# Performance work log

Hardware: AMD Instinct MI355X
Metric: run time of the kernel (lower is better)

The kernel has to match this reference:

```python
import jax, jax.numpy as jnp
import numpy as np

B, N, K, C, D, DP = 4, 4096, 32, 3, 64, 128  # batch, npoint, nsample, xyz, feat, all_channel
DC = C + D + 2  # channels of dgf = pg|pf|dg|df
ALPHA = 0.2


def setup_inputs() -> dict:
    key = jax.random.key(0)
    ks = jax.random.split(key, 10)
    g = jax.random.normal(ks[0], (B, N, C), jnp.float32)
    f = jax.random.normal(ks[1], (B, N, D), jnp.float32)
    gn = jax.random.normal(ks[2], (B, N, K, C), jnp.float32)
    fn = jax.random.normal(ks[3], (B, N, K, D), jnp.float32)
    nfn = jax.random.normal(ks[4], (B, N, K, DP), jnp.float32)
    # learned params: attention matrix a (xavier-uniform in torch), 1x1 conv2d (DC->DP), 1x1 conv1d (DP->DP)
    lim_a = float(1.414 * np.sqrt(6.0 / (DP + DP)))
    a = jax.random.uniform(ks[5], (DP, DP), jnp.float32, -lim_a, lim_a)
    w2 = jax.random.normal(ks[6], (DC, DP), jnp.float32) * 0.05
    b2 = jax.random.normal(ks[7], (DP,), jnp.float32) * 0.01
    w1 = jax.random.normal(ks[8], (DP, DP), jnp.float32) * 0.05
    b1 = jax.random.normal(ks[9], (DP,), jnp.float32) * 0.01
    return {"g": g, "f": f, "gn": gn, "fn": fn, "nfn": nfn,
            "a": a, "w2": w2, "b2": b2, "w1": w1, "b1": b1,
            "b": B, "n": N, "k": K, "c": DP, "nc": DP}


def reference(g, f, gn, fn, nfn, a, w2, b2, w1, b1, b, n, k, c, nc):
    # relative coords / features: [B,N,K,C], [B,N,K,D]
    pg = g[:, :, None, :] - gn
    pf = f[:, :, None, :] - fn
    # diso(A, B) = sqrt(sum((A-B)^2, -1))[..., None]
    dg = jnp.sqrt(jnp.sum((pg - gn) ** 2, axis=-1, keepdims=True))  # [B,N,K,1]
    df = jnp.sqrt(jnp.sum((pf - fn) ** 2, axis=-1, keepdims=True))  # [B,N,K,1]
    dgf = jnp.concatenate([pg, pf, dg, df], axis=-1)                 # [B,N,K,DC]
    # 1x1 conv2d projection (computed but unused by the original forward; returned here)
    disf = jnp.einsum("bnkd,de->bnke", dgf, w2) + b2                # [B,N,K,DP]
    # GAT-style attention over the neighbor axis
    e = jax.nn.leaky_relu(jnp.einsum("bnkd,de->bnke", nfn, a), ALPHA)
    att = jax.nn.softmax(e, axis=2)  # softmax over nsample; dropout is identity in eval mode
    pooled = jnp.sum(att * nfn, axis=2)                              # [B,N,DP]
    out = jnp.einsum("bnd,dc->bnc", pooled, w1) + b1                 # [B,N,c]
    return out, disf
```

## Files before the change

kernel.cpp:

```cpp
#include <hip/hip_runtime.h>
#include <math.h>

constexpr int Bv = 4;
constexpr int Nv = 4096;
constexpr int Kv = 32;
constexpr int Cv = 3;
constexpr int Dv = 64;
constexpr int DP = 128;
constexpr float ALPHA = 0.2f;

typedef __bf16 bf16x8 __attribute__((ext_vector_type(8)));
typedef float  f32x4  __attribute__((ext_vector_type(4)));
typedef short  s16x8  __attribute__((ext_vector_type(8)));

__device__ __forceinline__ short f2bf(float x) {
    unsigned u = __float_as_uint(x);
    unsigned r = (u + 0x7FFFu + ((u >> 16) & 1u)) >> 16;
    return (short)r;
}
__device__ __forceinline__ float bf2f(short s) {
    return __uint_as_float(((unsigned)(unsigned short)s) << 16);
}
__device__ __forceinline__ int swz(int row, int bytecol) {
    return row * 256 + (bytecol ^ ((row & 7) << 4));
}
__device__ __forceinline__ bf16x8 ld_frag(const char* base, int row, int bytecol) {
    return __builtin_bit_cast(bf16x8, *(const s16x8*)(base + swz(row, bytecol)));
}

__global__ __launch_bounds__(256) void prep_kernel(
    const float* __restrict__ a, const float* __restrict__ w2,
    const float* __restrict__ w1,
    short* __restrict__ aT_swz, short* __restrict__ w2T_swz,
    float* __restrict__ w1T)
{
    const int idx = blockIdx.x * 256 + threadIdx.x;
    const int c = idx >> 7, s = idx & 127;
    const int off = (c * 256 + ((s * 2) ^ ((c & 7) << 4))) >> 1;
    aT_swz[off] = f2bf(a[(size_t)s * DP + c]);
    float v = 0.f;
    if (s < 64)       v = w2[(size_t)(3 + s) * DP + c];
    else if (s < 67)  v = w2[(size_t)(s - 64) * DP + c];
    else if (s == 67) v = w2[(size_t)67 * DP + c];
    else if (s == 68) v = w2[(size_t)68 * DP + c];
    w2T_swz[off] = f2bf(v);
    w1T[(size_t)c * DP + s] = w1[(size_t)s * DP + c];
}

__global__ __launch_bounds__(256, 2) void attn_kernel(
    const float* __restrict__ nfn,
    const short* __restrict__ aT_swz,
    const float* __restrict__ w1T,
    const float* __restrict__ b1,
    float* __restrict__ out)
{
    __shared__ __align__(16) char s_nfn[128 * 256];
    __shared__ __align__(16) char s_aT[128 * 256];
    __shared__ float s_pool[4][DP];

    const int bn0 = blockIdx.x * 4;
    const int t = threadIdx.x;

    {
        const s16x8* src = (const s16x8*)aT_swz;
        s16x8* dst = (s16x8*)s_aT;
#pragma unroll
        for (int i = 0; i < 8; ++i) dst[t + 256 * i] = src[t + 256 * i];
    }
    {
        const int r = t >> 1, h = t & 1;
        const float4* src = (const float4*)(nfn + ((size_t)bn0 * 32 + r) * DP + h * 64);
#pragma unroll
        for (int cc = 0; cc < 8; ++cc) {
            float4 v0 = src[2 * cc], v1 = src[2 * cc + 1];
            s16x8 v = { f2bf(v0.x), f2bf(v0.y), f2bf(v0.z), f2bf(v0.w),
                        f2bf(v1.x), f2bf(v1.y), f2bf(v1.z), f2bf(v1.w) };
            *(s16x8*)(s_nfn + swz(r, h * 128 + cc * 16)) = v;
        }
    }
    __syncthreads();

    const int w = t >> 6, lane = t & 63;
    const int wr = w >> 1, wc = w & 1;
    const int lg = lane >> 4, lm = lane & 15;

    f32x4 acc[4][4];
#pragma unroll
    for (int mt = 0; mt < 4; ++mt)
#pragma unroll
        for (int nt = 0; nt < 4; ++nt) acc[mt][nt] = (f32x4)0.f;

#pragma unroll
    for (int kt = 0; kt < 4; ++kt) {
        bf16x8 afr[4], bfr[4];
#pragma unroll
        for (int mt = 0; mt < 4; ++mt)
            afr[mt] = ld_frag(s_nfn, wr * 64 + mt * 16 + lm, kt * 64 + lg * 16);
#pragma unroll
        for (int nt = 0; nt < 4; ++nt)
            bfr[nt] = ld_frag(s_aT, wc * 64 + nt * 16 + lm, kt * 64 + lg * 16);
#pragma unroll
        for (int mt = 0; mt < 4; ++mt)
#pragma unroll
            for (int nt = 0; nt < 4; ++nt)
                acc[mt][nt] = __builtin_amdgcn_mfma_f32_16x16x32_bf16(
                    afr[mt], bfr[nt], acc[mt][nt], 0, 0, 0);
    }

#pragma unroll
    for (int gp = 0; gp < 2; ++gp) {
#pragma unroll
        for (int nt = 0; nt < 4; ++nt) {
            float v[8];
            float m = -1e30f;
#pragma unroll
            for (int tt = 0; tt < 2; ++tt)
#pragma unroll
                for (int rg = 0; rg < 4; ++rg) {
                    float e = acc[2 * gp + tt][nt][rg];
                    e = e > 0.f ? e : ALPHA * e;
                    v[tt * 4 + rg] = e;
                    m = fmaxf(m, e);
                }
            m = fmaxf(m, __shfl_xor(m, 16));
            m = fmaxf(m, __shfl_xor(m, 32));
            float s = 0.f, p = 0.f;
            const int col = wc * 64 + nt * 16 + lm;
#pragma unroll
            for (int tt = 0; tt < 2; ++tt)
#pragma unroll
                for (int rg = 0; rg < 4; ++rg) {
                    float ex = __expf(v[tt * 4 + rg] - m);
                    s += ex;
                    const int row = wr * 64 + (2 * gp + tt) * 16 + lg * 4 + rg;
                    p += ex * bf2f(*(const short*)(s_nfn + swz(row, col * 2)));
                }
            s += __shfl_xor(s, 16); s += __shfl_xor(s, 32);
            p += __shfl_xor(p, 16); p += __shfl_xor(p, 32);
            if (lg == 0) s_pool[wr * 2 + gp][col] = p / s;
        }
    }
    __syncthreads();

    {
        const int c = t & 127, g2 = t >> 7;
        const float4* w1r = (const float4*)(w1T + (size_t)c * DP);
#pragma unroll
        for (int gg = 0; gg < 2; ++gg) {
            const int g = g2 + 2 * gg;
            const float4* pr = (const float4*)(&s_pool[g][0]);
            float acc2 = b1[c];
#pragma unroll
            for (int j = 0; j < 32; ++j) {
                float4 wv = w1r[j];
                float4 pv = pr[j];
                acc2 = fmaf(pv.x, wv.x, acc2);
                acc2 = fmaf(pv.y, wv.y, acc2);
                acc2 = fmaf(pv.z, wv.z, acc2);
                acc2 = fmaf(pv.w, wv.w, acc2);
            }
            out[((size_t)bn0 + g) * DP + c] = acc2;
        }
    }
}

__global__ __launch_bounds__(256, 2) void disf_kernel(
    const float* __restrict__ g,
    const float* __restrict__ f,
    const float* __restrict__ gn,
    const float* __restrict__ fn,
    const short* __restrict__ w2T_swz,
    const float* __restrict__ b2,
    float* __restrict__ disf)
{
    __shared__ __align__(16) char s_dgf[128 * 256];
    __shared__ __align__(16) char s_w2T[128 * 256];

    const int bn0 = blockIdx.x * 4;
    const int t = threadIdx.x;

    {
        const s16x8* src = (const s16x8*)w2T_swz;
        s16x8* dst = (s16x8*)s_w2T;
#pragma unroll
        for (int i = 0; i < 8; ++i) dst[t + 256 * i] = src[t + 256 * i];
    }
    {
        const int r = t >> 1, h = t & 1;
        const int grp = r >> 5, k = r & 31;
        const size_t bn = bn0 + grp;
        const float4* fp  = (const float4*)(f + bn * Dv + h * 32);
        const float4* fnp = (const float4*)(fn + (bn * Kv + k) * Dv + h * 32);
        float sq = 0.f;
#pragma unroll
        for (int cc = 0; cc < 4; ++cc) {
            float4 f0 = fp[2 * cc],  f1 = fp[2 * cc + 1];
            float4 n0 = fnp[2 * cc], n1 = fnp[2 * cc + 1];
            float p0 = f0.x - n0.x, p1 = f0.y - n0.y, p2 = f0.z - n0.z, p3 = f0.w - n0.w;
            float p4 = f1.x - n1.x, p5 = f1.y - n1.y, p6 = f1.z - n1.z, p7 = f1.w - n1.w;
            float q;
            q = p0 - n0.x; sq += q * q;  q = p1 - n0.y; sq += q * q;
            q = p2 - n0.z; sq += q * q;  q = p3 - n0.w; sq += q * q;
            q = p4 - n1.x; sq += q * q;  q = p5 - n1.y; sq += q * q;
            q = p6 - n1.z; sq += q * q;  q = p7 - n1.w; sq += q * q;
            s16x8 v = { f2bf(p0), f2bf(p1), f2bf(p2), f2bf(p3),
                        f2bf(p4), f2bf(p5), f2bf(p6), f2bf(p7) };
            *(s16x8*)(s_dgf + swz(r, h * 64 + cc * 16)) = v;
        }
        sq += __shfl_xor(sq, 1);
        if (h == 0) {
            const float* gp  = g + bn * Cv;
            const float* gnp = gn + (bn * Kv + k) * Cv;
            float p0 = gp[0] - gnp[0], p1 = gp[1] - gnp[1], p2 = gp[2] - gnp[2];
            float q0 = p0 - gnp[0], q1 = p1 - gnp[1], q2 = p2 - gnp[2];
            float dg = sqrtf(q0 * q0 + q1 * q1 + q2 * q2);
            float df = sqrtf(sq);
            s16x8 z = (s16x8)(short)0;
            s16x8 head = z;
            head[0] = f2bf(p0); head[1] = f2bf(p1); head[2] = f2bf(p2);
            head[3] = f2bf(dg); head[4] = f2bf(df);
            *(s16x8*)(s_dgf + swz(r, 128)) = head;
            *(s16x8*)(s_dgf + swz(r, 144)) = z;
            *(s16x8*)(s_dgf + swz(r, 160)) = z;
            *(s16x8*)(s_dgf + swz(r, 176)) = z;
        }
    }
    __syncthreads();

    const int w = t >> 6, lane = t & 63;
    const int wr = w >> 1, wc = w & 1;
    const int lg = lane >> 4, lm = lane & 15;

    f32x4 acc[4][4];
#pragma unroll
    for (int mt = 0; mt < 4; ++mt)
#pragma unroll
        for (int nt = 0; nt < 4; ++nt) acc[mt][nt] = (f32x4)0.f;

#pragma unroll
    for (int kt = 0; kt < 3; ++kt) {
        bf16x8 afr[4], bfr[4];
#pragma unroll
        for (int mt = 0; mt < 4; ++mt)
            afr[mt] = ld_frag(s_dgf, wr * 64 + mt * 16 + lm, kt * 64 + lg * 16);
#pragma unroll
        for (int nt = 0; nt < 4; ++nt)
            bfr[nt] = ld_frag(s_w2T, wc * 64 + nt * 16 + lm, kt * 64 + lg * 16);
#pragma unroll
        for (int mt = 0; mt < 4; ++mt)
#pragma unroll
            for (int nt = 0; nt < 4; ++nt)
                acc[mt][nt] = __builtin_amdgcn_mfma_f32_16x16x32_bf16(
                    afr[mt], bfr[nt], acc[mt][nt], 0, 0, 0);
    }

    float b2v[4];
#pragma unroll
    for (int nt = 0; nt < 4; ++nt) b2v[nt] = b2[wc * 64 + nt * 16 + lm];

#pragma unroll
    for (int mt = 0; mt < 4; ++mt) {
#pragma unroll
        for (int rg = 0; rg < 4; ++rg) {
            const int row = wr * 64 + mt * 16 + lg * 4 + rg;
            float* dst = disf + ((size_t)bn0 * 32 + row) * DP + wc * 64 + lm;
#pragma unroll
            for (int nt = 0; nt < 4; ++nt)
                dst[nt * 16] = acc[mt][nt][rg] + b2v[nt];
        }
    }
}

extern "C" void kernel_launch(void* const* d_in, const int* in_sizes, int n_in,
                              void* d_out, int out_size, void* d_ws, size_t ws_size,
                              hipStream_t stream) {
    (void)in_sizes; (void)n_in; (void)out_size; (void)ws_size;

    const float* g   = (const float*)d_in[0];
    const float* f   = (const float*)d_in[1];
    const float* gn  = (const float*)d_in[2];
    const float* fn  = (const float*)d_in[3];
    const float* nfn = (const float*)d_in[4];
    const float* a   = (const float*)d_in[5];
    const float* w2  = (const float*)d_in[6];
    const float* b2  = (const float*)d_in[7];
    const float* w1  = (const float*)d_in[8];
    const float* b1  = (const float*)d_in[9];

    float* out  = (float*)d_out;
    float* disf = out + (size_t)Bv * Nv * DP;

    short* aT_swz  = (short*)d_ws;
    short* w2T_swz = aT_swz + 128 * 128;
    float* w1T     = (float*)(w2T_swz + 128 * 128);

    prep_kernel<<<64, 256, 0, stream>>>(a, w2, w1, aT_swz, w2T_swz, w1T);

    dim3 grid(Bv * Nv / 4);
    attn_kernel<<<grid, 256, 0, stream>>>(nfn, aT_swz, w1T, b1, out);
    disf_kernel<<<grid, 256, 0, stream>>>(g, f, gn, fn, w2T_swz, b2, disf);
}
```

Measured before the change: 802.5 us.

## Restructure attention and disf kernels to per-wave 32x32 MFMA with register prefetch

Each wave now processes one neighbor group at a time using 32x32x16 bf16 MFMAs and prefetches the next group's inputs into registers while computing the current one, replacing block-wide 16x16 tiles and a sync. The output projection is split into a separate MFMA kernel that reads pooled features staged in a scratch region carved from the tail of the disf output buffer. The projection now runs in bf16 instead of fp32 FMAs. This aims to overlap global loads with compute and reduce LDS traffic, but adds a kernel launch and a dependency on disf_kernel overwriting the scratch later.

```diff
diff --git a/kernel.cpp b/kernel.cpp
--- a/kernel.cpp
+++ b/kernel.cpp
@@ -8,10 +8,12 @@
 constexpr int Dv = 64;
 constexpr int DP = 128;
 constexpr float ALPHA = 0.2f;
+constexpr int NG = Bv * Nv;
 
 typedef __bf16 bf16x8 __attribute__((ext_vector_type(8)));
-typedef float  f32x4  __attribute__((ext_vector_type(4)));
+typedef float  f32x16 __attribute__((ext_vector_type(16)));
 typedef short  s16x8  __attribute__((ext_vector_type(8)));
+typedef short  s16x4  __attribute__((ext_vector_type(4)));
 
 __device__ __forceinline__ short f2bf(float x) {
     unsigned u = __float_as_uint(x);
@@ -32,34 +34,31 @@
     const float* __restrict__ a, const float* __restrict__ w2,
     const float* __restrict__ w1,
     short* __restrict__ aT_swz, short* __restrict__ w2T_swz,
-    float* __restrict__ w1T)
+    short* __restrict__ w1T_swz)
 {
     const int idx = blockIdx.x * 256 + threadIdx.x;
     const int c = idx >> 7, s = idx & 127;
     const int off = (c * 256 + ((s * 2) ^ ((c & 7) << 4))) >> 1;
-    aT_swz[off] = f2bf(a[(size_t)s * DP + c]);
+    aT_swz[off]  = f2bf(a[(size_t)s * DP + c]);
+    w1T_swz[off] = f2bf(w1[(size_t)s * DP + c]);
     float v = 0.f;
     if (s < 64)       v = w2[(size_t)(3 + s) * DP + c];
     else if (s < 67)  v = w2[(size_t)(s - 64) * DP + c];
     else if (s == 67) v = w2[(size_t)67 * DP + c];
     else if (s == 68) v = w2[(size_t)68 * DP + c];
     w2T_swz[off] = f2bf(v);
-    w1T[(size_t)c * DP + s] = w1[(size_t)s * DP + c];
-}
-
-__global__ __launch_bounds__(256, 2) void attn_kernel(
+}
+
+__global__ __launch_bounds__(256, 2) void attn_core(
     const float* __restrict__ nfn,
     const short* __restrict__ aT_swz,
-    const float* __restrict__ w1T,
-    const float* __restrict__ b1,
-    float* __restrict__ out)
+    float* __restrict__ pooled)
 {
-    __shared__ __align__(16) char s_nfn[128 * 256];
     __shared__ __align__(16) char s_aT[128 * 256];
-    __shared__ float s_pool[4][DP];
-
-    const int bn0 = blockIdx.x * 4;
-    const int t = threadIdx.x;
+    __shared__ __align__(16) char s_buf[4][32 * 256];
+
+    const int t = threadIdx.x, w = t >> 6, l = t & 63;
+    const int lg = l >> 5, lG = l & 31;
 
     {
         const s16x8* src = (const s16x8*)aT_swz;
@@ -67,101 +66,128 @@
 #pragma unroll
         for (int i = 0; i < 8; ++i) dst[t + 256 * i] = src[t + 256 * i];
     }
-    {
-        const int r = t >> 1, h = t & 1;
-        const float4* src = (const float4*)(nfn + ((size_t)bn0 * 32 + r) * DP + h * 64);
-#pragma unroll
-        for (int cc = 0; cc < 8; ++cc) {
-            float4 v0 = src[2 * cc], v1 = src[2 * cc + 1];
-            s16x8 v = { f2bf(v0.x), f2bf(v0.y), f2bf(v0.z), f2bf(v0.w),
-                        f2bf(v1.x), f2bf(v1.y), f2bf(v1.z), f2bf(v1.w) };
-            *(s16x8*)(s_nfn + swz(r, h * 128 + cc * 16)) = v;
-        }
-    }
     __syncthreads();
 
-    const int w = t >> 6, lane = t & 63;
-    const int wr = w >> 1, wc = w & 1;
-    const int lg = lane >> 4, lm = lane & 15;
-
-    f32x4 acc[4][4];
-#pragma unroll
-    for (int mt = 0; mt < 4; ++mt)
-#pragma unroll
-        for (int nt = 0; nt < 4; ++nt) acc[mt][nt] = (f32x4)0.f;
-
-#pragma unroll
-    for (int kt = 0; kt < 4; ++kt) {
-        bf16x8 afr[4], bfr[4];
-#pragma unroll
-        for (int mt = 0; mt < 4; ++mt)
-            afr[mt] = ld_frag(s_nfn, wr * 64 + mt * 16 + lm, kt * 64 + lg * 16);
-#pragma unroll
-        for (int nt = 0; nt < 4; ++nt)
-            bfr[nt] = ld_frag(s_aT, wc * 64 + nt * 16 + lm, kt * 64 + lg * 16);
-#pragma unroll
-        for (int mt = 0; mt < 4; ++mt)
-#pragma unroll
-            for (int nt = 0; nt < 4; ++nt)
-                acc[mt][nt] = __builtin_amdgcn_mfma_f32_16x16x32_bf16(
-                    afr[mt], bfr[nt], acc[mt][nt], 0, 0, 0);
-    }
-
-#pragma unroll
-    for (int gp = 0; gp < 2; ++gp) {
+    char* buf = s_buf[w];
+    const int g0 = blockIdx.x * 16 + w * 4;
+
+    float4 rv[16];
+    {
+        const float4* src = (const float4*)(nfn + (size_t)g0 * Kv * DP);
+#pragma unroll
+        for (int j = 0; j < 16; ++j) rv[j] = src[j * 64 + l];
+    }
+
+    for (int it = 0; it < 4; ++it) {
+        const int g = g0 + it;
+#pragma unroll
+        for (int j = 0; j < 16; ++j) {
+            s16x4 v = { f2bf(rv[j].x), f2bf(rv[j].y), f2bf(rv[j].z), f2bf(rv[j].w) };
+            *(s16x4*)(buf + swz(j * 2 + lg, lG * 8)) = v;
+        }
+        if (it < 3) {
+            const float4* src = (const float4*)(nfn + (size_t)(g + 1) * Kv * DP);
+#pragma unroll
+            for (int j = 0; j < 16; ++j) rv[j] = src[j * 64 + l];
+        }
+
+        bf16x8 afr[8];
+#pragma unroll
+        for (int k = 0; k < 8; ++k) afr[k] = ld_frag(buf, lG, k * 32 + lg * 16);
+
+        f32x16 acc[4];
+#pragma unroll
+        for (int nt = 0; nt < 4; ++nt) acc[nt] = (f32x16)0.f;
+#pragma unroll
+        for (int k = 0; k < 8; ++k)
+#pragma unroll
+            for (int nt = 0; nt < 4; ++nt) {
+                bf16x8 bfr = ld_frag(s_aT, nt * 32 + lG, k * 32 + lg * 16);
+                acc[nt] = __builtin_amdgcn_mfma_f32_32x32x16_bf16(
+                    afr[k], bfr, acc[nt], 0, 0, 0);
+            }
+
 #pragma unroll
         for (int nt = 0; nt < 4; ++nt) {
-            float v[8];
+            float v[16];
             float m = -1e30f;
 #pragma unroll
-            for (int tt = 0; tt < 2; ++tt)
-#pragma unroll
-                for (int rg = 0; rg < 4; ++rg) {
-                    float e = acc[2 * gp + tt][nt][rg];
-                    e = e > 0.f ? e : ALPHA * e;
-                    v[tt * 4 + rg] = e;
-                    m = fmaxf(m, e);
-                }
-            m = fmaxf(m, __shfl_xor(m, 16));
+            for (int r = 0; r < 16; ++r) {
+                float e = acc[nt][r];
+                e = e > 0.f ? e : ALPHA * e;
+                v[r] = e;
+                m = fmaxf(m, e);
+            }
             m = fmaxf(m, __shfl_xor(m, 32));
             float s = 0.f, p = 0.f;
-            const int col = wc * 64 + nt * 16 + lm;
-#pragma unroll
-            for (int tt = 0; tt < 2; ++tt)
-#pragma unroll
-                for (int rg = 0; rg < 4; ++rg) {
-                    float ex = __expf(v[tt * 4 + rg] - m);
-                    s += ex;
-                    const int row = wr * 64 + (2 * gp + tt) * 16 + lg * 4 + rg;
-                    p += ex * bf2f(*(const short*)(s_nfn + swz(row, col * 2)));
-                }
-            s += __shfl_xor(s, 16); s += __shfl_xor(s, 32);
-            p += __shfl_xor(p, 16); p += __shfl_xor(p, 32);
-            if (lg == 0) s_pool[wr * 2 + gp][col] = p / s;
-        }
+            const int col = nt * 32 + lG;
+#pragma unroll
+            for (int r = 0; r < 16; ++r) {
+                float ex = __expf(v[r] - m);
+                s += ex;
+                const int row = (r & 3) + 8 * (r >> 2) + 4 * lg;
+                p += ex * bf2f(*(const short*)(buf + swz(row, col * 2)));
+            }
+            s += __shfl_xor(s, 32);
+            p += __shfl_xor(p, 32);
+            if (lg == 0) pooled[(size_t)g * DP + col] = p / s;
+        }
+    }
+}
+
+__global__ __launch_bounds__(256, 2) void out_proj(
+    const float* __restrict__ pooled, const short* __restrict__ w1T_swz,
+    const float* __restrict__ b1, float* __restrict__ out)
+{
+    __shared__ __align__(16) char s_w1[128 * 256];
+    __shared__ __align__(16) char s_buf[4][32 * 256];
+
+    const int t = threadIdx.x, w = t >> 6, l = t & 63;
+    const int lg = l >> 5, lG = l & 31;
+    {
+        const s16x8* src = (const s16x8*)w1T_swz;
+        s16x8* dst = (s16x8*)s_w1;
+#pragma unroll
+        for (int i = 0; i < 8; ++i) dst[t + 256 * i] = src[t + 256 * i];
     }
     __syncthreads();
 
-    {
-        const int c = t & 127, g2 = t >> 7;
-        const float4* w1r = (const float4*)(w1T + (size_t)c * DP);
-#pragma unroll
-        for (int gg = 0; gg < 2; ++gg) {
-            const int g = g2 + 2 * gg;
-            const float4* pr = (const float4*)(&s_pool[g][0]);
-            float acc2 = b1[c];
-#pragma unroll
-            for (int j = 0; j < 32; ++j) {
-                float4 wv = w1r[j];
-                float4 pv = pr[j];
-                acc2 = fmaf(pv.x, wv.x, acc2);
-                acc2 = fmaf(pv.y, wv.y, acc2);
-                acc2 = fmaf(pv.z, wv.z, acc2);
-                acc2 = fmaf(pv.w, wv.w, acc2);
-            }
-            out[((size_t)bn0 + g) * DP + c] = acc2;
-        }
-    }
+    char* buf = s_buf[w];
+    const int grp = blockIdx.x * 4 + w;
+    {
+        const float4* src = (const float4*)(pooled + (size_t)grp * 32 * DP);
+#pragma unroll
+        for (int j = 0; j < 16; ++j) {
+            float4 v4 = src[j * 64 + l];
+            s16x4 v = { f2bf(v4.x), f2bf(v4.y), f2bf(v4.z), f2bf(v4.w) };
+            *(s16x4*)(buf + swz(j * 2 + lg, lG * 8)) = v;
+        }
+    }
+    bf16x8 afr[8];
+#pragma unroll
+    for (int k = 0; k < 8; ++k) afr[k] = ld_frag(buf, lG, k * 32 + lg * 16);
+
+    f32x16 acc[4];
+#pragma unroll
+    for (int nt = 0; nt < 4; ++nt) acc[nt] = (f32x16)0.f;
+#pragma unroll
+    for (int k = 0; k < 8; ++k)
+#pragma unroll
+        for (int nt = 0; nt < 4; ++nt) {
+            bf16x8 bfr = ld_frag(s_w1, nt * 32 + lG, k * 32 + lg * 16);
+            acc[nt] = __builtin_amdgcn_mfma_f32_32x32x16_bf16(
+                afr[k], bfr, acc[nt], 0, 0, 0);
+        }
+    float b1v[4];
+#pragma unroll
+    for (int nt = 0; nt < 4; ++nt) b1v[nt] = b1[nt * 32 + lG];
+#pragma unroll
+    for (int nt = 0; nt < 4; ++nt)
+#pragma unroll
+        for (int r = 0; r < 16; ++r) {
+            const int row = (r & 3) + 8 * (r >> 2) + 4 * lg;
+            out[((size_t)grp * 32 + row) * DP + nt * 32 + lG] = acc[nt][r] + b1v[nt];
+        }
 }
 
 __global__ __launch_bounds__(256, 2) void disf_kernel(
@@ -173,31 +199,48 @@
     const float* __restrict__ b2,
     float* __restrict__ disf)
 {
-    __shared__ __align__(16) char s_dgf[128 * 256];
-    __shared__ __align__(16) char s_w2T[128 * 256];
-
-    const int bn0 = blockIdx.x * 4;
-    const int t = threadIdx.x;
-
+    __shared__ __align__(16) char s_w2[128 * 256];
+    __shared__ __align__(16) char s_buf[4][32 * 256];
+
+    const int t = threadIdx.x, w = t >> 6, l = t & 63;
+    const int lg = l >> 5, lG = l & 31;
     {
         const s16x8* src = (const s16x8*)w2T_swz;
-        s16x8* dst = (s16x8*)s_w2T;
+        s16x8* dst = (s16x8*)s_w2;
 #pragma unroll
         for (int i = 0; i < 8; ++i) dst[t + 256 * i] = src[t + 256 * i];
     }
-    {
-        const int r = t >> 1, h = t & 1;
-        const int grp = r >> 5, k = r & 31;
-        const size_t bn = bn0 + grp;
-        const float4* fp  = (const float4*)(f + bn * Dv + h * 32);
-        const float4* fnp = (const float4*)(fn + (bn * Kv + k) * Dv + h * 32);
+    __syncthreads();
+
+    char* buf = s_buf[w];
+    const int g0 = blockIdx.x * 16 + w * 4;
+
+    float b2v[4];
+#pragma unroll
+    for (int nt = 0; nt < 4; ++nt) b2v[nt] = b2[nt * 32 + lG];
+
+    float4 rf[8], rn[8];
+    float gv0, gv1, gv2, gn0, gn1, gn2;
+    {
+        const float4* fp  = (const float4*)(f + (size_t)g0 * Dv + lg * 32);
+        const float4* fnp = (const float4*)(fn + ((size_t)g0 * Kv + lG) * Dv + lg * 32);
+#pragma unroll
+        for (int j = 0; j < 8; ++j) { rf[j] = fp[j]; rn[j] = fnp[j]; }
+        const float* gp  = g + (size_t)g0 * Cv;
+        const float* gnp = gn + ((size_t)g0 * Kv + lG) * Cv;
+        gv0 = gp[0]; gv1 = gp[1]; gv2 = gp[2];
+        gn0 = gnp[0]; gn1 = gnp[1]; gn2 = gnp[2];
+    }
+
+    for (int it = 0; it < 4; ++it) {
+        const int bn = g0 + it;
         float sq = 0.f;
 #pragma unroll
-        for (int cc = 0; cc < 4; ++cc) {
-            float4 f0 = fp[2 * cc],  f1 = fp[2 * cc + 1];
-            float4 n0 = fnp[2 * cc], n1 = fnp[2 * cc + 1];
-            float p0 = f0.x - n0.x, p1 = f0.y - n0.y, p2 = f0.z - n0.z, p3 = f0.w - n0.w;
-            float p4 = f1.x - n1.x, p5 = f1.y - n1.y, p6 = f1.z - n1.z, p7 = f1.w - n1.w;
+        for (int j = 0; j < 4; ++j) {
+            float4 a0 = rf[2 * j], a1 = rf[2 * j + 1];
+            float4 n0 = rn[2 * j], n1 = rn[2 * j + 1];
+            float p0 = a0.x - n0.x, p1 = a0.y - n0.y, p2 = a0.z - n0.z, p3 = a0.w - n0.w;
+            float p4 = a1.x - n1.x, p5 = a1.y - n1.y, p6 = a1.z - n1.z, p7 = a1.w - n1.w;
             float q;
             q = p0 - n0.x; sq += q * q;  q = p1 - n0.y; sq += q * q;
             q = p2 - n0.z; sq += q * q;  q = p3 - n0.w; sq += q * q;
@@ -205,69 +248,56 @@
             q = p6 - n1.z; sq += q * q;  q = p7 - n1.w; sq += q * q;
             s16x8 v = { f2bf(p0), f2bf(p1), f2bf(p2), f2bf(p3),
                         f2bf(p4), f2bf(p5), f2bf(p6), f2bf(p7) };
-            *(s16x8*)(s_dgf + swz(r, h * 64 + cc * 16)) = v;
-        }
-        sq += __shfl_xor(sq, 1);
-        if (h == 0) {
-            const float* gp  = g + bn * Cv;
-            const float* gnp = gn + (bn * Kv + k) * Cv;
-            float p0 = gp[0] - gnp[0], p1 = gp[1] - gnp[1], p2 = gp[2] - gnp[2];
-            float q0 = p0 - gnp[0], q1 = p1 - gnp[1], q2 = p2 - gnp[2];
+            *(s16x8*)(buf + swz(lG, lg * 64 + j * 16)) = v;
+        }
+        sq += __shfl_xor(sq, 32);
+        if (lg == 0) {
+            float p0 = gv0 - gn0, p1 = gv1 - gn1, p2 = gv2 - gn2;
+            float q0 = p0 - gn0, q1 = p1 - gn1, q2 = p2 - gn2;
             float dg = sqrtf(q0 * q0 + q1 * q1 + q2 * q2);
             float df = sqrtf(sq);
             s16x8 z = (s16x8)(short)0;
             s16x8 head = z;
             head[0] = f2bf(p0); head[1] = f2bf(p1); head[2] = f2bf(p2);
             head[3] = f2bf(dg); head[4] = f2bf(df);
-            *(s16x8*)(s_dgf + swz(r, 128)) = head;
-            *(s16x8*)(s_dgf + swz(r, 144)) = z;
-            *(s16x8*)(s_dgf + swz(r, 160)) = z;
-            *(s16x8*)(s_dgf + swz(r, 176)) = z;
-        }
-    }
-    __syncthreads();
-
-    const int w = t >> 6, lane = t & 63;
-    const int wr = w >> 1, wc = w & 1;
-    const int lg = lane >> 4, lm = lane & 15;
-
-    f32x4 acc[4][4];
-#pragma unroll
-    for (int mt = 0; mt < 4; ++mt)
-#pragma unroll
-        for (int nt = 0; nt < 4; ++nt) acc[mt][nt] = (f32x4)0.f;
-
-#pragma unroll
-    for (int kt = 0; kt < 3; ++kt) {
-        bf16x8 afr[4], bfr[4];
-#pragma unroll
-        for (int mt = 0; mt < 4; ++mt)
-            afr[mt] = ld_frag(s_dgf, wr * 64 + mt * 16 + lm, kt * 64 + lg * 16);
+            *(s16x8*)(buf + swz(lG, 128)) = head;
+            *(s16x8*)(buf + swz(lG, 144)) = z;
+            *(s16x8*)(buf + swz(lG, 160)) = z;
+            *(s16x8*)(buf + swz(lG, 176)) = z;
+        }
+        if (it < 3) {
+            const float4* fp  = (const float4*)(f + (size_t)(bn + 1) * Dv + lg * 32);
+            const float4* fnp = (const float4*)(fn + ((size_t)(bn + 1) * Kv + lG) * Dv + lg * 32);
+#pragma unroll
+            for (int j = 0; j < 8; ++j) { rf[j] = fp[j]; rn[j] = fnp[j]; }
+            const float* gp  = g + (size_t)(bn + 1) * Cv;
+            const float* gnp = gn + ((size_t)(bn + 1) * Kv + lG) * Cv;
+            gv0 = gp[0]; gv1 = gp[1]; gv2 = gp[2];
+            gn0 = gnp[0]; gn1 = gnp[1]; gn2 = gnp[2];
+        }
+
+        bf16x8 afr[6];
+#pragma unroll
+        for (int k = 0; k < 6; ++k) afr[k] = ld_frag(buf, lG, k * 32 + lg * 16);
+
+        f32x16 acc[4];
+#pragma unroll
+        for (int nt = 0; nt < 4; ++nt) acc[nt] = (f32x16)0.f;
+#pragma unroll
+        for (int k = 0; k < 6; ++k)
+#pragma unroll
+            for (int nt = 0; nt < 4; ++nt) {
+                bf16x8 bfr = ld_frag(s_w2, nt * 32 + lG, k * 32 + lg * 16);
+                acc[nt] = __builtin_amdgcn_mfma_f32_32x32x16_bf16(
+                    afr[k], bfr, acc[nt], 0, 0, 0);
+            }
 #pragma unroll
         for (int nt = 0; nt < 4; ++nt)
-            bfr[nt] = ld_frag(s_w2T, wc * 64 + nt * 16 + lm, kt * 64 + lg * 16);
-#pragma unroll
-        for (int mt = 0; mt < 4; ++mt)
-#pragma unroll
-            for (int nt = 0; nt < 4; ++nt)
-                acc[mt][nt] = __builtin_amdgcn_mfma_f32_16x16x32_bf16(
-                    afr[mt], bfr[nt], acc[mt][nt], 0, 0, 0);
-    }
-
-    float b2v[4];
-#pragma unroll
-    for (int nt = 0; nt < 4; ++nt) b2v[nt] = b2[wc * 64 + nt * 16 + lm];
-
-#pragma unroll
-    for (int mt = 0; mt < 4; ++mt) {
-#pragma unroll
-        for (int rg = 0; rg < 4; ++rg) {
-            const int row = wr * 64 + mt * 16 + lg * 4 + rg;
-            float* dst = disf + ((size_t)bn0 * 32 + row) * DP + wc * 64 + lm;
-#pragma unroll
-            for (int nt = 0; nt < 4; ++nt)
-                dst[nt * 16] = acc[mt][nt][rg] + b2v[nt];
-        }
+#pragma unroll
+            for (int r = 0; r < 16; ++r) {
+                const int row = (r & 3) + 8 * (r >> 2) + 4 * lg;
+                disf[((size_t)bn * Kv + row) * DP + nt * 32 + lG] = acc[nt][r] + b2v[nt];
+            }
     }
 }
 
@@ -288,15 +318,15 @@
     const float* b1  = (const float*)d_in[9];
 
     float* out  = (float*)d_out;
-    float* disf = out + (size_t)Bv * Nv * DP;
+    float* disf = out + (size_t)NG * DP;
+    float* pooled = disf + (size_t)NG * Kv * DP - (size_t)NG * DP;
 
     short* aT_swz  = (short*)d_ws;
     short* w2T_swz = aT_swz + 128 * 128;
-    float* w1T     = (float*)(w2T_swz + 128 * 128);
-
-    prep_kernel<<<64, 256, 0, stream>>>(a, w2, w1, aT_swz, w2T_swz, w1T);
-
-    dim3 grid(Bv * Nv / 4);
-    attn_kernel<<<grid, 256, 0, stream>>>(nfn, aT_swz, w1T, b1, out);
-    disf_kernel<<<grid, 256, 0, stream>>>(g, f, gn, fn, w2T_swz, b2, disf);
-}
+    short* w1T_swz = w2T_swz + 128 * 128;
+
+    prep_kernel<<<64, 256, 0, stream>>>(a, w2, w1, aT_swz, w2T_swz, w1T_swz);
+    attn_core<<<1024, 256, 0, stream>>>(nfn, aT_swz, pooled);
+    out_proj<<<128, 256, 0, stream>>>(pooled, w1T_swz, b1, out);
+    disf_kernel<<<1024, 256, 0, stream>>>(g, f, gn, fn, w2T_swz, b2, disf);
+}
```

Measured after the change: 705.9 us. 1.14x faster.
